# Kernel optimization log

Hardware: AMD Instinct MI355X
Metric: run time of the kernel (lower is better)

The kernel has to match this reference:

```python
import jax, jax.numpy as jnp
import numpy as np

PRIOR_VAR = 0.01
NUM_HEADS = 12
EMBED_DIM = 768


def kl_regularizer(mu, logvar):
    kl_loss = (jnp.log(PRIOR_VAR) - 1.0 - logvar
               + jax.nn.softplus(logvar) / PRIOR_VAR
               + jnp.square(mu) / PRIOR_VAR)
    return 0.5 * jnp.mean(kl_loss)


def linear_vdp(mu_in, Sigma_in, w_mu, w_sigma):
    # mu_in, Sigma_in: [..., Din]; w_mu: [Din, Dout]; w_sigma: [Dout]
    mu_out = mu_in @ w_mu
    kl = kl_regularizer(w_mu, w_sigma)
    W_Sigma = jax.nn.softplus(w_sigma)                      # [Dout]
    din = w_mu.shape[0]
    # w_t_Sigma_i_w: w scaled by sqrt(Din)
    w_scaled = w_mu / jnp.sqrt(jnp.float32(din))
    Sigma_1 = Sigma_in @ (w_scaled * w_scaled)              # [..., Dout]
    # x_Sigma_w_x_T: x scaled by Din
    x = mu_in / jnp.float32(din)
    xx_t = jnp.sum(x * x, axis=-1, keepdims=True)
    Sigma_2 = xx_t * W_Sigma
    # tr_Sigma_w_Sigma_in
    Sigma_3 = jnp.sum(Sigma_in, axis=-1, keepdims=True) * W_Sigma / jnp.float32(w_mu.shape[-1])
    Sigma_out = jax.nn.softplus(Sigma_1 + Sigma_2 + Sigma_3)
    return mu_out, Sigma_out, kl


def split_heads(x, B, H, d):
    # [B, S, E] -> [B, H, S, d]
    return x.reshape(B, -1, H, d).transpose(0, 2, 1, 3)


def vdp_attention(mu_q, sg_q, mu_k, sg_k, mu_v, sg_v):
    d = jnp.float32(mu_k.shape[-1])
    sq = jnp.sqrt(d)
    mu_score = jnp.einsum('bhqd,bhkd->bhqk', mu_q, mu_k)
    a = jnp.einsum('bhqd,bhkd->bhqk', mu_q * mu_q / d, sg_k)
    b = jnp.einsum('bhid,bhjd->bhij', mu_k * mu_k / d, sg_q)  # TF matmul(key.., query.., transpose_b)
    c = jnp.einsum('bhqd,bhkd->bhqk', sg_q / sq, sg_k / sq)
    sigma_score = a + b + c
    mu_weights = jax.nn.softmax(mu_score / sq, axis=-1)
    wdim = jnp.float32(mu_weights.shape[-1])
    grad = jnp.square(mu_weights - mu_weights * mu_weights)
    Sigma_weights = grad * (sigma_score / d) / wdim
    mu_out = jnp.einsum('bhqk,bhkd->bhqd', mu_weights, mu_v)
    dterm = jnp.einsum('bhqk,bhkd->bhqd', mu_weights * mu_weights / wdim, sg_v)
    eterm = jnp.einsum('bhqk,bhkd->bhqd', Sigma_weights, mu_v * mu_v / wdim)
    fterm = jnp.einsum('bhqk,bhkd->bhqd', Sigma_weights / jnp.sqrt(wdim), sg_v / jnp.sqrt(wdim))
    out_sigma = jax.nn.softplus(dterm + eterm + fterm)
    return mu_out, out_sigma


def forward(mu_inputs, sigma_inputs, wq_mu, wq_sigma, wk_mu, wk_sigma,
            wv_mu, wv_sigma, wo_mu, wo_sigma):
    B = mu_inputs.shape[0]
    H = NUM_HEADS
    d = EMBED_DIM // H
    # VDP_Dropout with Training=False is identity
    mu_q, sg_q, kl_q = linear_vdp(mu_inputs, sigma_inputs, wq_mu, wq_sigma)
    mu_k, sg_k, kl_k = linear_vdp(mu_inputs, sigma_inputs, wk_mu, wk_sigma)
    mu_v, sg_v, kl_v = linear_vdp(mu_inputs, sigma_inputs, wv_mu, wv_sigma)
    mu_q, sg_q = split_heads(mu_q, B, H, d), split_heads(sg_q, B, H, d)
    mu_k, sg_k = split_heads(mu_k, B, H, d), split_heads(sg_k, B, H, d)
    mu_v, sg_v = split_heads(mu_v, B, H, d), split_heads(sg_v, B, H, d)
    mu_att, sg_att = vdp_attention(mu_q, sg_q, mu_k, sg_k, mu_v, sg_v)
    mu_cat = mu_att.transpose(0, 2, 1, 3).reshape(B, -1, EMBED_DIM)
    sg_cat = sg_att.transpose(0, 2, 1, 3).reshape(B, -1, EMBED_DIM)
    mu_out, Sigma_out, kl_c = linear_vdp(mu_cat, sg_cat, wo_mu, wo_sigma)
    Sigma_out = jax.nn.softplus(Sigma_out)
    kl = kl_q + kl_k + kl_v + kl_c
    return mu_out, Sigma_out, kl


def setup_inputs() -> dict:
    key = jax.random.key(0)
    ks = jax.random.split(key, 12)
    B, S, E = 4, 1024, EMBED_DIM
    glorot_std = np.sqrt(2.0 / (E + E)).astype(np.float32)
    def wsig(k):
        return jax.random.uniform(k, (E,), jnp.float32, -4.6, -2.25)
    return {
        'mu_inputs': jax.random.normal(ks[0], (B, S, E), jnp.float32),
        'sigma_inputs': jax.random.uniform(ks[1], (B, S, E), jnp.float32),
        'wq_mu': jax.random.normal(ks[2], (E, E), jnp.float32) * glorot_std,
        'wq_sigma': wsig(ks[3]),
        'wk_mu': jax.random.normal(ks[4], (E, E), jnp.float32) * glorot_std,
        'wk_sigma': wsig(ks[5]),
        'wv_mu': jax.random.normal(ks[6], (E, E), jnp.float32) * glorot_std,
        'wv_sigma': wsig(ks[7]),
        'wo_mu': jax.random.normal(ks[8], (E, E), jnp.float32) * glorot_std,
        'wo_sigma': wsig(ks[9]),
    }


def reference(mu_inputs, sigma_inputs, wq_mu, wq_sigma, wk_mu, wk_sigma,
              wv_mu, wv_sigma, wo_mu, wo_sigma):
    return forward(mu_inputs, sigma_inputs, wq_mu, wq_sigma, wk_mu, wk_sigma,
                   wv_mu, wv_sigma, wo_mu, wo_sigma)
```

## Files before the change

kernel.cpp:

```cpp
#include <hip/hip_runtime.h>
#include <math.h>

#define E 768
#define NTOK 4096

typedef __attribute__((ext_vector_type(8))) __bf16 bf16x8;
typedef __attribute__((ext_vector_type(4))) float f32x4;
typedef unsigned int u32;
typedef unsigned short u16;

#define BFN ((size_t)NTOK * E)
#define WFN ((size_t)E * E)
#define QSC 1.4901161193847656e-08f
#define C2E 0.18033688011112042f

__device__ __forceinline__ float sp_f(float x) {
    return fmaxf(x, 0.f) + log1pf(__expf(-fabsf(x)));
}
__device__ __forceinline__ u16 f2bf(float f) {
    u32 u = __float_as_uint(f);
    u += 0x7fffu + ((u >> 16) & 1u);
    return (u16)(u >> 16);
}
__device__ __forceinline__ u32 pk2(float a, float b) {
    return (u32)f2bf(a) | ((u32)f2bf(b) << 16);
}
__device__ __forceinline__ u32 cvtpk(float a, float b) {
    u32 r; asm("v_cvt_pk_bf16_f32 %0, %1, %2" : "=v"(r) : "v"(a), "v"(b)); return r;
}
__device__ __forceinline__ float ex2(float x) {
    float r; asm("v_exp_f32 %0, %1" : "=v"(r) : "v"(x)); return r;
}
__device__ __forceinline__ float lg2(float x) {
    float r; asm("v_log_f32 %0, %1" : "=v"(r) : "v"(x)); return r;
}
__device__ __forceinline__ float bfl(u32 u) { return __uint_as_float(u << 16); }
__device__ __forceinline__ float bfh(u32 u) { return __uint_as_float(u & 0xffff0000u); }

#define GLL16(gp, lp) __builtin_amdgcn_global_load_lds( \
    (const __attribute__((address_space(1))) u32*)(gp), \
    (__attribute__((address_space(3))) u32*)(lp), 16, 0, 0)

__global__ void prep_kernel(const float* __restrict__ wqs, const float* __restrict__ wks,
                            const float* __restrict__ wvs, const float* __restrict__ wos,
                            float* __restrict__ spws, float* __restrict__ kl_out)
{
    int i = blockIdx.x * 256 + threadIdx.x;
    if (i < 4 * E) {
        const float* src;
        int j;
        if (i < E)            { src = wqs; j = i; }
        else if (i < 2 * E)   { src = wks; j = i - E; }
        else if (i < 3 * E)   { src = wvs; j = i - 2 * E; }
        else                  { src = wos; j = i - 3 * E; }
        spws[i] = sp_f(src[j]);
    }
    if (i == 4 * E) *kl_out = 2.f * (logf(0.01f) - 1.f);
}

__global__ __launch_bounds__(128) void convstats_kernel(
    const float* __restrict__ mu, const float* __restrict__ sg,
    u16* __restrict__ Xmu, u16* __restrict__ Xsg,
    float* __restrict__ rmu2, float* __restrict__ rsg)
{
    const int n = blockIdx.x, tid = threadIdx.x;
    float s1 = 0.f, s2 = 0.f;
    if (tid < 96) {
        size_t o = (size_t)n * E + tid * 8;
        float4 a0 = *(const float4*)(mu + o), a1 = *(const float4*)(mu + o + 4);
        float4 b0 = *(const float4*)(sg + o), b1 = *(const float4*)(sg + o + 4);
        *(uint4*)(Xmu + o) = make_uint4(pk2(a0.x, a0.y), pk2(a0.z, a0.w), pk2(a1.x, a1.y), pk2(a1.z, a1.w));
        *(uint4*)(Xsg + o) = make_uint4(pk2(b0.x, b0.y), pk2(b0.z, b0.w), pk2(b1.x, b1.y), pk2(b1.z, b1.w));
        s1 = a0.x*a0.x + a0.y*a0.y + a0.z*a0.z + a0.w*a0.w + a1.x*a1.x + a1.y*a1.y + a1.z*a1.z + a1.w*a1.w;
        s2 = b0.x + b0.y + b0.z + b0.w + b1.x + b1.y + b1.z + b1.w;
    }
    for (int off = 32; off; off >>= 1) {
        s1 += __shfl_xor(s1, off);
        s2 += __shfl_xor(s2, off);
    }
    __shared__ float r1[2], r2[2];
    if ((tid & 63) == 0) { r1[tid >> 6] = s1; r2[tid >> 6] = s2; }
    __syncthreads();
    if (tid == 0) { rmu2[n] = r1[0] + r1[1]; rsg[n] = r2[0] + r2[1]; }
}

__global__ __launch_bounds__(128) void rowstats_bf16_kernel(
    const u16* __restrict__ mu, const u16* __restrict__ sg,
    float* __restrict__ rmu2, float* __restrict__ rsg)
{
    const int n = blockIdx.x, tid = threadIdx.x;
    float s1 = 0.f, s2 = 0.f;
    if (tid < 96) {
        uint4 um = *(const uint4*)(mu + (size_t)n * E + tid * 8);
        uint4 us = *(const uint4*)(sg + (size_t)n * E + tid * 8);
        u32 ua[4] = {um.x, um.y, um.z, um.w};
        u32 ub[4] = {us.x, us.y, us.z, us.w};
#pragma unroll
        for (int j = 0; j < 4; ++j) {
            float a0 = bfl(ua[j]), a1 = bfh(ua[j]);
            s1 += a0 * a0 + a1 * a1;
            s2 += bfl(ub[j]) + bfh(ub[j]);
        }
    }
    for (int off = 32; off; off >>= 1) {
        s1 += __shfl_xor(s1, off);
        s2 += __shfl_xor(s2, off);
    }
    __shared__ float r1[2], r2[2];
    if ((tid & 63) == 0) { r1[tid >> 6] = s1; r2[tid >> 6] = s2; }
    __syncthreads();
    if (tid == 0) { rmu2[n] = r1[0] + r1[1]; rsg[n] = r2[0] + r2[1]; }
}

__global__ void transpose_w_kernel(const float* __restrict__ W,
                                   u16* __restrict__ Wt, u16* __restrict__ W2t)
{
    __shared__ float T[32][33];
    const int j0 = blockIdx.x * 32, k0 = blockIdx.y * 32;
    const int tid = threadIdx.x;
    const int r = tid >> 3, c = (tid & 7) * 4;
    float4 v = *(const float4*)(W + (size_t)(k0 + r) * E + j0 + c);
    T[r][c] = v.x; T[r][c + 1] = v.y; T[r][c + 2] = v.z; T[r][c + 3] = v.w;
    __syncthreads();
    const int j = tid >> 3, kc = (tid & 7) * 4;
    float w0 = T[kc][j], w1 = T[kc + 1][j], w2 = T[kc + 2][j], w3 = T[kc + 3][j];
    size_t o = (size_t)(j0 + j) * E + k0 + kc;
    *(uint2*)(Wt + o) = make_uint2(pk2(w0, w1), pk2(w2, w3));
    const float s = 1.f / 768.f;
    *(uint2*)(W2t + o) = make_uint2(pk2(w0 * w0 * s, w1 * w1 * s), pk2(w2 * w2 * s, w3 * w3 * s));
}

template<int MODE>
__global__ __launch_bounds__(256, 3) void linear_fused(
    const u16* __restrict__ Am, const u16* __restrict__ As,
    const u16* __restrict__ Wt, const u16* __restrict__ W2t,
    const float* __restrict__ spws, const float* __restrict__ rmu2, const float* __restrict__ rsg,
    float* __restrict__ mu_out, float* __restrict__ sg_out, u16* __restrict__ QKVB)
{
    __shared__ __align__(16) u16 L[24576];

    const int wgid = blockIdx.x;
    const int NW = (MODE == 1) ? 144 : 48;
    const int NB = (MODE == 1) ? 36 : 12;
    const int swz = (wgid & 7) * NW + (wgid >> 3);
    const int m_blk = swz / NB, n_blk = swz % NB;
    const int m0 = m_blk * 128, col0 = n_blk * 64;
    const int tid = threadIdx.x, wv = tid >> 6, lane = tid & 63;
    const int g = lane >> 4, q15 = lane & 15;

    const u16* sp_[12];
#pragma unroll
    for (int j = 0; j < 12; ++j) {
        int ch = j * 256 + tid;
        int arr = (ch < 1024) ? 0 : (ch < 2048) ? 1 : (ch < 2560) ? 2 : 3;
        int local = ch - ((arr == 0) ? 0 : (arr == 1) ? 1024 : (arr == 2) ? 2048 : 2560);
        int r = local >> 3, c = local & 7;
        int cs = (c ^ (r & 7)) * 8;
        const u16* base = (arr == 0) ? (Am + (size_t)(m0 + r) * E) :
                          (arr == 1) ? (As + (size_t)(m0 + r) * E) :
                          (arr == 2) ? (Wt + (size_t)(col0 + r) * E) :
                                       (W2t + (size_t)(col0 + r) * E);
        sp_[j] = base + cs;
    }

    f32x4 acc1[2][4], acc2[2][4];
#pragma unroll
    for (int mt = 0; mt < 2; ++mt)
#pragma unroll
        for (int nt = 0; nt < 4; ++nt) {
            acc1[mt][nt] = (f32x4){0.f, 0.f, 0.f, 0.f};
            acc2[mt][nt] = (f32x4){0.f, 0.f, 0.f, 0.f};
        }

    for (int t = 0; t < 12; ++t) {
#pragma unroll
        for (int j = 0; j < 12; ++j)
            GLL16(sp_[j] + t * 64, (u16*)((char*)L + j * 4096 + wv * 1024));
        __syncthreads();
#pragma unroll
        for (int kk = 0; kk < 2; ++kk) {
            bf16x8 am[2], asg[2];
#pragma unroll
            for (int mt = 0; mt < 2; ++mt) {
                int r = wv * 32 + mt * 16 + q15;
                int c = ((kk * 4 + g) ^ (r & 7)) * 8;
                am[mt]  = *(const bf16x8*)&L[(r << 6) + c];
                asg[mt] = *(const bf16x8*)&L[8192 + (r << 6) + c];
            }
#pragma unroll
            for (int nt = 0; nt < 4; ++nt) {
                int rb = nt * 16 + q15;
                int cb = ((kk * 4 + g) ^ (rb & 7)) * 8;
                bf16x8 bw = *(const bf16x8*)&L[16384 + (rb << 6) + cb];
                bf16x8 b2 = *(const bf16x8*)&L[20480 + (rb << 6) + cb];
                acc1[0][nt] = __builtin_amdgcn_mfma_f32_16x16x32_bf16(am[0], bw, acc1[0][nt], 0, 0, 0);
                acc1[1][nt] = __builtin_amdgcn_mfma_f32_16x16x32_bf16(am[1], bw, acc1[1][nt], 0, 0, 0);
                acc2[0][nt] = __builtin_amdgcn_mfma_f32_16x16x32_bf16(asg[0], b2, acc2[0][nt], 0, 0, 0);
                acc2[1][nt] = __builtin_amdgcn_mfma_f32_16x16x32_bf16(asg[1], b2, acc2[1][nt], 0, 0, 0);
            }
        }
        __syncthreads();
    }

    const float inv2 = 1.f / (768.f * 768.f), invd = 1.f / 768.f;
    float rr[2][4];
#pragma unroll
    for (int mt = 0; mt < 2; ++mt)
#pragma unroll
        for (int r = 0; r < 4; ++r) {
            int row = m0 + wv * 32 + mt * 16 + g * 4 + r;
            rr[mt][r] = rmu2[row] * inv2 + rsg[row] * invd;
        }

    if (MODE == 0) {
#pragma unroll
        for (int mt = 0; mt < 2; ++mt)
#pragma unroll
            for (int nt = 0; nt < 4; ++nt)
#pragma unroll
                for (int r = 0; r < 4; ++r) {
                    int row = m0 + wv * 32 + mt * 16 + g * 4 + r;
                    int col = col0 + nt * 16 + q15;
                    float mu = acc1[mt][nt][r];
                    float sg = sp_f(sp_f(acc2[mt][nt][r] + rr[mt][r] * spws[col]));
                    mu_out[(size_t)row * E + col] = mu;
                    sg_out[(size_t)row * E + col] = sg;
                }
    } else {
        const int proj = n_blk / 12, h = n_blk % 12;
        if (proj < 2) {
            u16* b0 = QKVB + (size_t)(proj * 3 + 0) * BFN;
            u16* b1 = QKVB + (size_t)(proj * 3 + 1) * BFN;
            u16* b2 = QKVB + (size_t)(proj * 3 + 2) * BFN;
#pragma unroll
            for (int mt = 0; mt < 2; ++mt)
#pragma unroll
                for (int nt = 0; nt < 4; ++nt)
#pragma unroll
                    for (int r = 0; r < 4; ++r) {
                        int row = m0 + wv * 32 + mt * 16 + g * 4 + r;
                        int col = col0 + nt * 16 + q15;
                        float mu = acc1[mt][nt][r];
                        float sg = sp_f(acc2[mt][nt][r] + rr[mt][r] * spws[col]);
                        int bb = row >> 10, s = row & 1023, d = nt * 16 + q15;
                        size_t rb = ((size_t)(bb * 12 + h) << 16) + ((size_t)s << 6) + d;
                        b0[rb] = f2bf(mu);
                        b1[rb] = f2bf(sg);
                        b2[rb] = f2bf(proj == 0 ? (mu * mu + sg) * QSC : mu * mu * QSC);
                    }
        } else {
            float sgv[2][4][4];
#pragma unroll
            for (int mt = 0; mt < 2; ++mt)
#pragma unroll
                for (int nt = 0; nt < 4; ++nt)
#pragma unroll
                    for (int r = 0; r < 4; ++r) {
                        int col = col0 + nt * 16 + q15;
                        sgv[mt][nt][r] = sp_f(acc2[mt][nt][r] + rr[mt][r] * spws[col]);
                    }
            const int bb = m0 >> 10, s0 = m0 & 1023;
#pragma unroll
            for (int a = 0; a < 3; ++a) {
                __syncthreads();
#pragma unroll
                for (int mt = 0; mt < 2; ++mt)
#pragma unroll
                    for (int nt = 0; nt < 4; ++nt)
#pragma unroll
                        for (int r = 0; r < 4; ++r) {
                            float mu = acc1[mt][nt][r], sg = sgv[mt][nt][r];
                            float v = (a == 0) ? mu : (a == 1) ? sg * 0.0009765625f : mu * mu + sg;
                            L[(nt * 16 + q15) * 136 + wv * 32 + mt * 16 + g * 4 + r] = f2bf(v);
                        }
                __syncthreads();
                const int d = tid >> 2, sc = (tid & 3) * 32;
                u16* dst = QKVB + (size_t)(6 + a) * BFN;
                size_t ga = ((size_t)((bb * 12 + h) * 64 + d) << 10) + s0 + sc;
                *(uint4*)(dst + ga)      = *(const uint4*)&L[d * 136 + sc];
                *(uint4*)(dst + ga + 8)  = *(const uint4*)&L[d * 136 + sc + 8];
                *(uint4*)(dst + ga + 16) = *(const uint4*)&L[d * 136 + sc + 16];
                *(uint4*)(dst + ga + 24) = *(const uint4*)&L[d * 136 + sc + 24];
            }
        }
    }
}

#define PLB 12288
__global__ __launch_bounds__(256, 4) void vdp_attn5(
    const u16* __restrict__ Kmu, const u16* __restrict__ Ksg, const u16* __restrict__ Asq,
    const u16* __restrict__ Qmu, const u16* __restrict__ Q1v, const u16* __restrict__ Q2v,
    const u16* __restrict__ Vmu, const u16* __restrict__ Vsg, const u16* __restrict__ Vw2,
    u16* __restrict__ om, u16* __restrict__ osg)
{
    __shared__ __align__(16) u16 L[18432];

    const int wgid = blockIdx.x;
    const int seq = (wgid & 7) * 96 + (wgid >> 3);
    const int bh = seq >> 4, qt = seq & 15;
    const int tid = threadIdx.x, wv = tid >> 6, lane = tid & 63;
    const int g = lane >> 4, q15 = lane & 15;
    const size_t hb = (size_t)bh << 16;

    const size_t qoff = hb + (size_t)((qt * 64 + wv * 16 + q15) << 6) + g * 8;
    bf16x8 bq0 = *(const bf16x8*)(Qmu + qoff), bq1 = *(const bf16x8*)(Qmu + qoff + 32);
    bf16x8 b10 = *(const bf16x8*)(Q1v + qoff), b11 = *(const bf16x8*)(Q1v + qoff + 32);
    bf16x8 b20 = *(const bf16x8*)(Q2v + qoff), b21 = *(const bf16x8*)(Q2v + qoff + 32);

    const int sr = tid >> 3, sc8 = tid & 7;
    const size_t koffA = hb + (size_t)sr * 64 + ((sc8 ^ (sr & 7)) << 3);
    const size_t koffB = hb + (size_t)(sr + 32) * 64 + ((sc8 ^ ((sr + 32) & 7)) << 3);
    const int vr = tid >> 2, vc = tid & 3;
    const size_t voff = hb + (size_t)vr * 1024 + ((vc ^ (vr & 3)) << 3);

    float m2 = -3.0e38f;
    float lacc[4] = {0.f, 0.f, 0.f, 0.f};
    for (int t = 0; t < 16; ++t) {
        GLL16(Kmu + koffA + ((size_t)t << 12), &L[wv * 512]);
        GLL16(Kmu + koffB + ((size_t)t << 12), &L[2048 + wv * 512]);
        __syncthreads();
        f32x4 sc[4];
#pragma unroll
        for (int kt = 0; kt < 4; ++kt) sc[kt] = (f32x4){0.f, 0.f, 0.f, 0.f};
        __builtin_amdgcn_s_setprio(1);
#pragma unroll
        for (int kt = 0; kt < 4; ++kt) {
            int row = kt * 16 + q15, ra = row << 6;
            bf16x8 k0 = *(const bf16x8*)&L[ra + ((g ^ (row & 7)) << 3)];
            bf16x8 k1 = *(const bf16x8*)&L[ra + (((g + 4) ^ (row & 7)) << 3)];
            sc[kt] = __builtin_amdgcn_mfma_f32_16x16x32_bf16(k0, bq0, sc[kt], 0, 0, 0);
            sc[kt] = __builtin_amdgcn_mfma_f32_16x16x32_bf16(k1, bq1, sc[kt], 0, 0, 0);
        }
        __builtin_amdgcn_s_setprio(0);
        float t0 = fmaxf(fmaxf(sc[0][0], sc[0][1]), fmaxf(sc[0][2], sc[0][3]));
        float t1 = fmaxf(fmaxf(sc[1][0], sc[1][1]), fmaxf(sc[1][2], sc[1][3]));
        float t2 = fmaxf(fmaxf(sc[2][0], sc[2][1]), fmaxf(sc[2][2], sc[2][3]));
        float t3 = fmaxf(fmaxf(sc[3][0], sc[3][1]), fmaxf(sc[3][2], sc[3][3]));
        float tm = fmaxf(fmaxf(t0, t1), fmaxf(t2, t3)) * C2E;
        if (tm > m2 + 8.f) {
            float f = ex2(m2 - tm);
            lacc[0] *= f; lacc[1] *= f; lacc[2] *= f; lacc[3] *= f;
            m2 = tm;
        }
#pragma unroll
        for (int kt = 0; kt < 4; ++kt)
#pragma unroll
            for (int r = 0; r < 4; ++r)
                lacc[kt] += ex2(fmaf(sc[kt][r], C2E, -m2));
        __syncthreads();
    }
    float l = (lacc[0] + lacc[1]) + (lacc[2] + lacc[3]);
#pragma unroll
    for (int off = 16; off <= 32; off <<= 1) {
        float mo = __shfl_xor(m2, off), lo = __shfl_xor(l, off);
        float nm = fmaxf(m2, mo);
        l = l * ex2(m2 - nm) + lo * ex2(mo - nm);
        m2 = nm;
    }
    const float M = m2 + lg2(l);

    f32x4 accm[4], accd[4], acce[4];
#pragma unroll
    for (int nt = 0; nt < 4; ++nt) {
        accm[nt] = (f32x4){0.f, 0.f, 0.f, 0.f};
        accd[nt] = (f32x4){0.f, 0.f, 0.f, 0.f};
        acce[nt] = (f32x4){0.f, 0.f, 0.f, 0.f};
    }
    const int plw = PLB + wv * 1536;

    for (int t = 0; t < 32; ++t) {
        const size_t ka = (size_t)t << 11;
        const size_t va = (size_t)t << 5;
        GLL16(Kmu + koffA + ka, &L[0     + wv * 512]);
        GLL16(Ksg + koffA + ka, &L[2048  + wv * 512]);
        GLL16(Asq + koffA + ka, &L[4096  + wv * 512]);
        GLL16(Vmu + voff + va,  &L[6144  + wv * 512]);
        GLL16(Vsg + voff + va,  &L[8192  + wv * 512]);
        GLL16(Vw2 + voff + va,  &L[10240 + wv * 512]);
        __syncthreads();

        f32x4 sc[2], sgc[2];
#pragma unroll
        for (int kt = 0; kt < 2; ++kt) { sc[kt] = (f32x4){0.f,0.f,0.f,0.f}; sgc[kt] = (f32x4){0.f,0.f,0.f,0.f}; }
        __builtin_amdgcn_s_setprio(1);
#pragma unroll
        for (int kt = 0; kt < 2; ++kt) {
            int row = kt * 16 + q15, ra = row << 6;
            int ca = ((g ^ (row & 7)) << 3), cb = (((g + 4) ^ (row & 7)) << 3);
            sc[kt]  = __builtin_amdgcn_mfma_f32_16x16x32_bf16(*(const bf16x8*)&L[ra + ca],        bq0, sc[kt],  0, 0, 0);
            sc[kt]  = __builtin_amdgcn_mfma_f32_16x16x32_bf16(*(const bf16x8*)&L[ra + cb],        bq1, sc[kt],  0, 0, 0);
            sgc[kt] = __builtin_amdgcn_mfma_f32_16x16x32_bf16(*(const bf16x8*)&L[2048 + ra + ca], b10, sgc[kt], 0, 0, 0);
            sgc[kt] = __builtin_amdgcn_mfma_f32_16x16x32_bf16(*(const bf16x8*)&L[2048 + ra + cb], b11, sgc[kt], 0, 0, 0);
            sgc[kt] = __builtin_amdgcn_mfma_f32_16x16x32_bf16(*(const bf16x8*)&L[4096 + ra + ca], b20, sgc[kt], 0, 0, 0);
            sgc[kt] = __builtin_amdgcn_mfma_f32_16x16x32_bf16(*(const bf16x8*)&L[4096 + ra + cb], b21, sgc[kt], 0, 0, 0);
        }
        __builtin_amdgcn_s_setprio(0);

#pragma unroll
        for (int kt = 0; kt < 2; ++kt) {
            float p[4], p2[4], sw[4];
#pragma unroll
            for (int r = 0; r < 4; ++r) {
                p[r] = ex2(fmaf(sc[kt][r], C2E, -M));
                p2[r] = p[r] * p[r];
                float gq = p[r] - p2[r];
                sw[r] = gq * gq * sgc[kt][r];
            }
            int ch = (kt << 1) + (g >> 1);
            int base = q15 * 32 + ((ch ^ (q15 & 3)) << 3) + ((g & 1) << 2);
#pragma unroll
            for (int rp = 0; rp < 4; rp += 2) {
                *(u32*)&L[plw + base + rp]        = cvtpk(p[rp],  p[rp + 1]);
                *(u32*)&L[plw + 512 + base + rp]  = cvtpk(p2[rp], p2[rp + 1]);
                *(u32*)&L[plw + 1024 + base + rp] = cvtpk(sw[rp], sw[rp + 1]);
            }
        }

        __builtin_amdgcn_s_setprio(1);
        {
            int pc = q15 * 32 + ((g ^ (q15 & 3)) << 3);
            bf16x8 pa  = *(const bf16x8*)&L[plw + pc];
            bf16x8 p2a = *(const bf16x8*)&L[plw + 512 + pc];
            bf16x8 swa = *(const bf16x8*)&L[plw + 1024 + pc];
#pragma unroll
            for (int nt = 0; nt < 4; ++nt) {
                int vi = (nt * 16 + q15) * 32 + ((g ^ (q15 & 3)) << 3);
                accm[nt] = __builtin_amdgcn_mfma_f32_16x16x32_bf16(pa,  *(const bf16x8*)&L[6144 + vi],  accm[nt], 0, 0, 0);
                accd[nt] = __builtin_amdgcn_mfma_f32_16x16x32_bf16(p2a, *(const bf16x8*)&L[8192 + vi],  accd[nt], 0, 0, 0);
                acce[nt] = __builtin_amdgcn_mfma_f32_16x16x32_bf16(swa, *(const bf16x8*)&L[10240 + vi], acce[nt], 0, 0, 0);
            }
        }
        __builtin_amdgcn_s_setprio(0);
        __syncthreads();
    }

    const int b_ = bh / 12, h_ = bh % 12;
#pragma unroll
    for (int nt = 0; nt < 4; ++nt)
#pragma unroll
        for (int r = 0; r < 4; ++r) {
            int srow = qt * 64 + wv * 16 + g * 4 + r;
            int d = nt * 16 + q15;
            size_t o = (size_t)(b_ * 1024 + srow) * E + h_ * 64 + d;
            om[o]  = f2bf(accm[nt][r]);
            osg[o] = f2bf(sp_f(accd[nt][r] + acce[nt][r]));
        }
}

__global__ void kl_kernel(const float* __restrict__ w0, const float* __restrict__ w1,
                          const float* __restrict__ w2, const float* __restrict__ w3,
                          const float* __restrict__ s0, const float* __restrict__ s1,
                          const float* __restrict__ s2, const float* __restrict__ s3,
                          float* __restrict__ kl_out)
{
    const int gid = blockIdx.x * 256 + threadIdx.x;
    const int gsz = gridDim.x * 256;
    float acc = 0.f;
    const float cw = 100.f / ((float)E * (float)E);
#pragma unroll
    for (int mm = 0; mm < 4; ++mm) {
        const float* w = (mm == 0) ? w0 : (mm == 1) ? w1 : (mm == 2) ? w2 : w3;
        const float* sv = (mm == 0) ? s0 : (mm == 1) ? s1 : (mm == 2) ? s2 : s3;
        for (int i = gid; i < E * E; i += gsz) { float x = w[i]; acc += x * x * cw; }
        for (int i = gid; i < E; i += gsz) { float x = sv[i]; acc += (-x + sp_f(x) * 100.f) * (1.f / (float)E); }
    }
    for (int off = 32; off; off >>= 1) acc += __shfl_xor(acc, off);
    __shared__ float r[4];
    int tid = threadIdx.x, w_ = tid >> 6;
    if ((tid & 63) == 0) r[w_] = acc;
    __syncthreads();
    if (tid == 0) atomicAdd(kl_out, 0.5f * (r[0] + r[1] + r[2] + r[3]));
}

extern "C" void kernel_launch(void* const* d_in, const int* in_sizes, int n_in,
                              void* d_out, int out_size, void* d_ws, size_t ws_size,
                              hipStream_t stream)
{
    const float* mu_in = (const float*)d_in[0];
    const float* sg_in = (const float*)d_in[1];
    const float* wq  = (const float*)d_in[2];
    const float* wqs = (const float*)d_in[3];
    const float* wk  = (const float*)d_in[4];
    const float* wks = (const float*)d_in[5];
    const float* wvp = (const float*)d_in[6];
    const float* wvs = (const float*)d_in[7];
    const float* wo  = (const float*)d_in[8];
    const float* wos = (const float*)d_in[9];

    float* out_mu = (float*)d_out;
    float* out_sg = out_mu + (size_t)NTOK * E;
    float* kl_out = out_mu + 2 * (size_t)NTOK * E;

    float* ws = (float*)d_ws;
    size_t off = 0;
    auto allocf = [&](size_t n) { float* p = ws + off; off += n; return p; };
    float* rmu2  = allocf(NTOK);
    float* rsgs  = allocf(NTOK);
    float* armu2 = allocf(NTOK);
    float* arsg  = allocf(NTOK);
    float* spws  = allocf(4 * E);

    u16* ub = (u16*)(ws + off);
    size_t uoff = 0;
    auto allocu = [&](size_t n) { u16* p = ub + uoff; uoff += n; return p; };
    u16* Xmu    = allocu(BFN);
    u16* Xsg    = allocu(BFN);
    u16* WtQKV  = allocu(3 * WFN);
    u16* W2tQKV = allocu(3 * WFN);
    u16* Wt3    = allocu(WFN);
    u16* W2t3   = allocu(WFN);
    u16* QKVB   = allocu(9 * BFN);
    u16* amu_b  = allocu(BFN);
    u16* asg_b  = allocu(BFN);
    (void)ws_size; (void)in_sizes; (void)n_in; (void)out_size;

    prep_kernel<<<13, 256, 0, stream>>>(wqs, wks, wvs, wos, spws, kl_out);
    convstats_kernel<<<NTOK, 128, 0, stream>>>(mu_in, sg_in, Xmu, Xsg, rmu2, rsgs);
    dim3 tgrid(24, 24);
    transpose_w_kernel<<<tgrid, 256, 0, stream>>>(wq,  WtQKV,           W2tQKV);
    transpose_w_kernel<<<tgrid, 256, 0, stream>>>(wk,  WtQKV + WFN,     W2tQKV + WFN);
    transpose_w_kernel<<<tgrid, 256, 0, stream>>>(wvp, WtQKV + 2 * WFN, W2tQKV + 2 * WFN);
    transpose_w_kernel<<<tgrid, 256, 0, stream>>>(wo,  Wt3,             W2t3);

    linear_fused<1><<<1152, 256, 0, stream>>>(Xmu, Xsg, WtQKV, W2tQKV, spws, rmu2, rsgs,
                                              nullptr, nullptr, QKVB);

    vdp_attn5<<<768, 256, 0, stream>>>(QKVB + 3 * BFN, QKVB + 4 * BFN, QKVB + 1 * BFN,
                                       QKVB + 0 * BFN, QKVB + 2 * BFN, QKVB + 5 * BFN,
                                       QKVB + 6 * BFN, QKVB + 7 * BFN, QKVB + 8 * BFN,
                                       amu_b, asg_b);

    rowstats_bf16_kernel<<<NTOK, 128, 0, stream>>>(amu_b, asg_b, armu2, arsg);
    linear_fused<0><<<384, 256, 0, stream>>>(amu_b, asg_b, Wt3, W2t3, spws + 3 * E, armu2, arsg,
                                             out_mu, out_sg, nullptr);

    kl_kernel<<<512, 256, 0, stream>>>(wq, wk, wvp, wo, wqs, wks, wvs, wos, kl_out);
}
```

Baseline: 240.0 us.

## Double-buffer K tiles in attention kernel and defer V-tile wait

Both attention passes now double-buffer the K-side tiles in LDS. The next tile's global-to-LDS load is issued before computing on the current one, so load latency overlaps the score MFMAs. V tiles load at the top of each iteration and are waited on with a partial vmcnt only before the PV MFMAs. The P staging buffer gets a padded stride (40) with a changed swizzle, writes widen to 64-bit, and the V and K swizzles are adjusted. LDS use rises to about 52KB, so launch bounds drop occupancy from 4 to 3 blocks per CU, and the hand-written vmcnt count depends on the order of loads the compiler emits.

```diff
diff --git a/kernel.cpp b/kernel.cpp
--- a/kernel.cpp
+++ b/kernel.cpp
@@ -286,14 +286,17 @@
     }
 }
 
-#define PLB 12288
-__global__ __launch_bounds__(256, 4) void vdp_attn5(
+#define KB0 0
+#define KB1 6144
+#define VB  12288
+#define PB  18432
+__global__ __launch_bounds__(256, 3) void vdp_attn6(
     const u16* __restrict__ Kmu, const u16* __restrict__ Ksg, const u16* __restrict__ Asq,
     const u16* __restrict__ Qmu, const u16* __restrict__ Q1v, const u16* __restrict__ Q2v,
     const u16* __restrict__ Vmu, const u16* __restrict__ Vsg, const u16* __restrict__ Vw2,
     u16* __restrict__ om, u16* __restrict__ osg)
 {
-    __shared__ __align__(16) u16 L[18432];
+    __shared__ __align__(16) u16 L[26112];
 
     const int wgid = blockIdx.x;
     const int seq = (wgid & 7) * 96 + (wgid >> 3);
@@ -309,23 +312,30 @@
 
     const int sr = tid >> 3, sc8 = tid & 7;
     const size_t koffA = hb + (size_t)sr * 64 + ((sc8 ^ (sr & 7)) << 3);
-    const size_t koffB = hb + (size_t)(sr + 32) * 64 + ((sc8 ^ ((sr + 32) & 7)) << 3);
+    const size_t koffB = hb + (size_t)(sr + 32) * 64 + ((sc8 ^ (sr & 7)) << 3);
     const int vr = tid >> 2, vc = tid & 3;
-    const size_t voff = hb + (size_t)vr * 1024 + ((vc ^ (vr & 3)) << 3);
+    const size_t voff = hb + (size_t)vr * 1024 + ((vc ^ ((vr >> 1) & 3)) << 3);
+
+    int cur = 0;
 
     float m2 = -3.0e38f;
     float lacc[4] = {0.f, 0.f, 0.f, 0.f};
+    GLL16(Kmu + koffA, &L[KB0 + wv * 512]);
+    GLL16(Kmu + koffB, &L[KB0 + 2048 + wv * 512]);
+    __syncthreads();
     for (int t = 0; t < 16; ++t) {
-        GLL16(Kmu + koffA + ((size_t)t << 12), &L[wv * 512]);
-        GLL16(Kmu + koffB + ((size_t)t << 12), &L[2048 + wv * 512]);
-        __syncthreads();
+        const int tn = (t < 15) ? t + 1 : 15;
+        const int nb = cur ? KB0 : KB1;
+        GLL16(Kmu + koffA + ((size_t)tn << 12), &L[nb + wv * 512]);
+        GLL16(Kmu + koffB + ((size_t)tn << 12), &L[nb + 2048 + wv * 512]);
+        const int kb = cur ? KB1 : KB0;
         f32x4 sc[4];
 #pragma unroll
         for (int kt = 0; kt < 4; ++kt) sc[kt] = (f32x4){0.f, 0.f, 0.f, 0.f};
         __builtin_amdgcn_s_setprio(1);
 #pragma unroll
         for (int kt = 0; kt < 4; ++kt) {
-            int row = kt * 16 + q15, ra = row << 6;
+            int row = kt * 16 + q15, ra = kb + (row << 6);
             bf16x8 k0 = *(const bf16x8*)&L[ra + ((g ^ (row & 7)) << 3)];
             bf16x8 k1 = *(const bf16x8*)&L[ra + (((g + 4) ^ (row & 7)) << 3)];
             sc[kt] = __builtin_amdgcn_mfma_f32_16x16x32_bf16(k0, bq0, sc[kt], 0, 0, 0);
@@ -348,6 +358,7 @@
             for (int r = 0; r < 4; ++r)
                 lacc[kt] += ex2(fmaf(sc[kt][r], C2E, -m2));
         __syncthreads();
+        cur ^= 1;
     }
     float l = (lacc[0] + lacc[1]) + (lacc[2] + lacc[3]);
 #pragma unroll
@@ -366,26 +377,34 @@
         accd[nt] = (f32x4){0.f, 0.f, 0.f, 0.f};
         acce[nt] = (f32x4){0.f, 0.f, 0.f, 0.f};
     }
-    const int plw = PLB + wv * 1536;
+    const int plw = PB + wv * 1920;
+
+    cur = 0;
+    GLL16(Kmu + koffA, &L[KB0 + 0    + wv * 512]);
+    GLL16(Ksg + koffA, &L[KB0 + 2048 + wv * 512]);
+    GLL16(Asq + koffA, &L[KB0 + 4096 + wv * 512]);
+    __syncthreads();
 
     for (int t = 0; t < 32; ++t) {
-        const size_t ka = (size_t)t << 11;
         const size_t va = (size_t)t << 5;
-        GLL16(Kmu + koffA + ka, &L[0     + wv * 512]);
-        GLL16(Ksg + koffA + ka, &L[2048  + wv * 512]);
-        GLL16(Asq + koffA + ka, &L[4096  + wv * 512]);
-        GLL16(Vmu + voff + va,  &L[6144  + wv * 512]);
-        GLL16(Vsg + voff + va,  &L[8192  + wv * 512]);
-        GLL16(Vw2 + voff + va,  &L[10240 + wv * 512]);
-        __syncthreads();
-
+        GLL16(Vmu + voff + va, &L[VB + 0    + wv * 512]);
+        GLL16(Vsg + voff + va, &L[VB + 2048 + wv * 512]);
+        GLL16(Vw2 + voff + va, &L[VB + 4096 + wv * 512]);
+        const int tn = (t < 31) ? t + 1 : 31;
+        const size_t ka = (size_t)tn << 11;
+        const int nb = cur ? KB0 : KB1;
+        GLL16(Kmu + koffA + ka, &L[nb + 0    + wv * 512]);
+        GLL16(Ksg + koffA + ka, &L[nb + 2048 + wv * 512]);
+        GLL16(Asq + koffA + ka, &L[nb + 4096 + wv * 512]);
+
+        const int kb = cur ? KB1 : KB0;
         f32x4 sc[2], sgc[2];
 #pragma unroll
         for (int kt = 0; kt < 2; ++kt) { sc[kt] = (f32x4){0.f,0.f,0.f,0.f}; sgc[kt] = (f32x4){0.f,0.f,0.f,0.f}; }
         __builtin_amdgcn_s_setprio(1);
 #pragma unroll
         for (int kt = 0; kt < 2; ++kt) {
-            int row = kt * 16 + q15, ra = row << 6;
+            int row = kt * 16 + q15, ra = kb + (row << 6);
             int ca = ((g ^ (row & 7)) << 3), cb = (((g + 4) ^ (row & 7)) << 3);
             sc[kt]  = __builtin_amdgcn_mfma_f32_16x16x32_bf16(*(const bf16x8*)&L[ra + ca],        bq0, sc[kt],  0, 0, 0);
             sc[kt]  = __builtin_amdgcn_mfma_f32_16x16x32_bf16(*(const bf16x8*)&L[ra + cb],        bq1, sc[kt],  0, 0, 0);
@@ -406,32 +425,36 @@
                 float gq = p[r] - p2[r];
                 sw[r] = gq * gq * sgc[kt][r];
             }
-            int ch = (kt << 1) + (g >> 1);
-            int base = q15 * 32 + ((ch ^ (q15 & 3)) << 3) + ((g & 1) << 2);
-#pragma unroll
-            for (int rp = 0; rp < 4; rp += 2) {
-                *(u32*)&L[plw + base + rp]        = cvtpk(p[rp],  p[rp + 1]);
-                *(u32*)&L[plw + 512 + base + rp]  = cvtpk(p2[rp], p2[rp + 1]);
-                *(u32*)&L[plw + 1024 + base + rp] = cvtpk(sw[rp], sw[rp + 1]);
-            }
-        }
+            int ch = (kt << 1) | (g >> 1);
+            int base = q15 * 40 + ((ch ^ ((q15 >> 1) & 3)) << 3) + ((g & 1) << 2);
+            *(uint2*)&L[plw + base]        = make_uint2(cvtpk(p[0],  p[1]),  cvtpk(p[2],  p[3]));
+            *(uint2*)&L[plw + 640 + base]  = make_uint2(cvtpk(p2[0], p2[1]), cvtpk(p2[2], p2[3]));
+            *(uint2*)&L[plw + 1280 + base] = make_uint2(cvtpk(sw[0], sw[1]), cvtpk(sw[2], sw[3]));
+        }
+
+        asm volatile("s_waitcnt vmcnt(3)" ::: "memory");
+        __builtin_amdgcn_sched_barrier(0);
+        __builtin_amdgcn_s_barrier();
+        __builtin_amdgcn_sched_barrier(0);
 
         __builtin_amdgcn_s_setprio(1);
         {
-            int pc = q15 * 32 + ((g ^ (q15 & 3)) << 3);
+            int pc = q15 * 40 + ((g ^ ((q15 >> 1) & 3)) << 3);
             bf16x8 pa  = *(const bf16x8*)&L[plw + pc];
-            bf16x8 p2a = *(const bf16x8*)&L[plw + 512 + pc];
-            bf16x8 swa = *(const bf16x8*)&L[plw + 1024 + pc];
+            bf16x8 p2a = *(const bf16x8*)&L[plw + 640 + pc];
+            bf16x8 swa = *(const bf16x8*)&L[plw + 1280 + pc];
 #pragma unroll
             for (int nt = 0; nt < 4; ++nt) {
-                int vi = (nt * 16 + q15) * 32 + ((g ^ (q15 & 3)) << 3);
-                accm[nt] = __builtin_amdgcn_mfma_f32_16x16x32_bf16(pa,  *(const bf16x8*)&L[6144 + vi],  accm[nt], 0, 0, 0);
-                accd[nt] = __builtin_amdgcn_mfma_f32_16x16x32_bf16(p2a, *(const bf16x8*)&L[8192 + vi],  accd[nt], 0, 0, 0);
-                acce[nt] = __builtin_amdgcn_mfma_f32_16x16x32_bf16(swa, *(const bf16x8*)&L[10240 + vi], acce[nt], 0, 0, 0);
+                int row = nt * 16 + q15;
+                int vi = (row << 5) + ((g ^ ((q15 >> 1) & 3)) << 3);
+                accm[nt] = __builtin_amdgcn_mfma_f32_16x16x32_bf16(pa,  *(const bf16x8*)&L[VB + vi],        accm[nt], 0, 0, 0);
+                accd[nt] = __builtin_amdgcn_mfma_f32_16x16x32_bf16(p2a, *(const bf16x8*)&L[VB + 2048 + vi], accd[nt], 0, 0, 0);
+                acce[nt] = __builtin_amdgcn_mfma_f32_16x16x32_bf16(swa, *(const bf16x8*)&L[VB + 4096 + vi], acce[nt], 0, 0, 0);
             }
         }
         __builtin_amdgcn_s_setprio(0);
         __syncthreads();
+        cur ^= 1;
     }
 
     const int b_ = bh / 12, h_ = bh % 12;
@@ -525,7 +548,7 @@
     linear_fused<1><<<1152, 256, 0, stream>>>(Xmu, Xsg, WtQKV, W2tQKV, spws, rmu2, rsgs,
                                               nullptr, nullptr, QKVB);
 
-    vdp_attn5<<<768, 256, 0, stream>>>(QKVB + 3 * BFN, QKVB + 4 * BFN, QKVB + 1 * BFN,
+    vdp_attn6<<<768, 256, 0, stream>>>(QKVB + 3 * BFN, QKVB + 4 * BFN, QKVB + 1 * BFN,
                                        QKVB + 0 * BFN, QKVB + 2 * BFN, QKVB + 5 * BFN,
                                        QKVB + 6 * BFN, QKVB + 7 * BFN, QKVB + 8 * BFN,
                                        amu_b, asg_b);
```

Measured after the change: 231.3 us. -3.6%, faster.
